# Kernel optimization log

Measured on AMD Instinct MI355X. Metric: run time of the kernel, lower is better.

## Reference

```python
import jax, jax.numpy as jnp
import numpy as np

N = 100000
H = 128
F_IN = 32
F_OUT = 16
NUM_GRAPHS = 64
NEG_SLOPE = 0.2


def setup_inputs() -> dict:
    key = jax.random.key(0)
    ks = jax.random.split(key, 16)
    inp = {
        'x': jax.random.normal(ks[0], (N, F_IN), dtype=jnp.float32),
        'edge_index': jax.random.randint(ks[1], (2, 1000000), 0, N, dtype=jnp.int32),
        'subgraph_edge_index': jax.random.randint(ks[2], (2, 1000000), 0, N, dtype=jnp.int32),
        'node_subnode_index': jax.random.randint(ks[3], (2, 200000), 0, N, dtype=jnp.int32),
        'subnode_node_index': jax.random.randint(ks[4], (2, 200000), 0, N, dtype=jnp.int32),
        'ground_node': jnp.arange(40000, dtype=jnp.int32),
        'subgraph_batch_index': jax.random.randint(ks[5], (60000,), 0, NUM_GRAPHS, dtype=jnp.int32),
        'batch_idx': jax.random.randint(ks[6], (40000,), 0, NUM_GRAPHS, dtype=jnp.int32),
    }
    s_in = 1.0 / np.sqrt(F_IN)
    s_h = 1.0 / np.sqrt(H)
    inp['emb_W'] = jax.random.uniform(ks[7], (F_IN, H), jnp.float32, -s_in, s_in)
    inp['emb_b'] = jax.random.uniform(ks[8], (H,), jnp.float32, -s_in, s_in)
    # 4 GATv2 layers (depth=1): lin_l, lin_r, att, bias per layer
    inp['Wl'] = jax.random.uniform(ks[9], (4, H, H), jnp.float32, -s_h, s_h)
    inp['Wr'] = jax.random.uniform(ks[10], (4, H, H), jnp.float32, -s_h, s_h)
    inp['att'] = jax.random.uniform(ks[11], (4, H), jnp.float32, -s_h, s_h)
    inp['bias'] = jax.random.uniform(ks[12], (4, H), jnp.float32, -s_h, s_h)
    inp['out_W'] = jax.random.uniform(ks[13], (H, F_OUT), jnp.float32, -s_h, s_h)
    inp['out_b'] = jax.random.uniform(ks[14], (F_OUT,), jnp.float32, -s_h, s_h)
    return inp


def _gatv2(x, ei, Wl, Wr, att, b):
    # add self loops (PyG GATv2Conv default add_self_loops=True)
    loops = jnp.broadcast_to(jnp.arange(N, dtype=ei.dtype)[None, :], (2, N))
    ei = jnp.concatenate([ei, loops], axis=1)
    src, dst = ei[0], ei[1]
    xl = x @ Wl  # source transform [N,H]
    xr = x @ Wr  # target transform [N,H]
    e = jax.nn.leaky_relu(xl[src] + xr[dst], NEG_SLOPE) @ att  # [E]
    m = jax.ops.segment_max(e, dst, num_segments=N)
    p = jnp.exp(e - m[dst])
    s = jax.ops.segment_sum(p, dst, num_segments=N)
    alpha = p / s[dst]
    out = jax.ops.segment_sum(alpha[:, None] * xl[src], dst, num_segments=N)
    return out + b


def reference(x, edge_index, subgraph_edge_index, node_subnode_index,
              subnode_node_index, ground_node, subgraph_batch_index, batch_idx,
              emb_W, emb_b, Wl, Wr, att, bias, out_W, out_b):
    h = x @ emb_W + emb_b
    eis = (edge_index, node_subnode_index, subgraph_edge_index, subnode_node_index)
    for i, ei in enumerate(eis):
        h = _gatv2(h, ei, Wl[i], Wr[i], att[i], bias[i])
    # global_add_pool over ground nodes
    pooled = jax.ops.segment_sum(h[ground_node], batch_idx, num_segments=NUM_GRAPHS)
    return pooled @ out_W + out_b
```

## Files before the change

kernel.cpp:

```cpp
#include <hip/hip_runtime.h>
#include <cstddef>


typedef __attribute__((ext_vector_type(8))) short bf16x8;
typedef __attribute__((ext_vector_type(4))) float f32x4;
typedef __attribute__((ext_vector_type(2))) float f32x2;

#define NSH   10
#define CHUNK 8192
#define POOLP 256

__device__ __forceinline__ unsigned short f2bf(float f) {
  unsigned int u = __float_as_uint(f);
  u += 0x7fffu + ((u >> 16) & 1u);
  return (unsigned short)(u >> 16);
}
__device__ __forceinline__ unsigned int pack2bf(float a, float b) {
  return (__float_as_uint(a) >> 16) | (__float_as_uint(b) & 0xFFFF0000u);
}
__device__ __forceinline__ float bf2f(short s) {
  return __uint_as_float(((unsigned int)(unsigned short)s) << 16);
}
__device__ __forceinline__ float2 unpk(unsigned int u) {
  return make_float2(__uint_as_float(u << 16),
                     __uint_as_float(u & 0xFFFF0000u));
}
__device__ __forceinline__ f32x2 unpk2(unsigned int u) {
  f32x2 r;
  r.x = __uint_as_float(u << 16);
  r.y = __uint_as_float(u & 0xFFFF0000u);
  return r;
}
__device__ __forceinline__ int dlog(int s) {
  int b = s >> 6, i = s & 63;
  return (b << 6) + ((i & 3) << 4) + (i >> 2);
}

__device__ __forceinline__ int lds_excl_scan(int* a, int len, int* aux, int tid)
{
  int g = (len + 255) >> 8;
  int lo = tid * g;
  int s = 0;
  for (int i = 0; i < g; ++i) { int idx = lo + i; if (idx < len) s += a[idx]; }
  aux[tid] = s;
  __syncthreads();
  for (int d = 1; d < 256; d <<= 1) {
    int v = (tid >= d) ? aux[tid - d] : 0;
    __syncthreads();
    aux[tid] += v;
    __syncthreads();
  }
  int run = aux[tid] - s;
  for (int i = 0; i < g; ++i) {
    int idx = lo + i;
    if (idx < len) { int t = a[idx]; a[idx] = run; run += t; }
  }
  int total = aux[255];
  __syncthreads();
  return total;
}

__device__ __forceinline__ void resolve_item(
    int id, int t1, int t2, int t3, int t4, int n,
    const int* s0, const int* s1, const int* s2, const int* s3,
    const int* d0, const int* d1, const int* d2, const int* d3,
    int& l, int& s, int& d, bool need_src)
{
  if (id < t4) {
    const int *sp, *dp; int e;
    if      (id < t1) { l = 0; e = id;      sp = s0; dp = d0; }
    else if (id < t2) { l = 1; e = id - t1; sp = s1; dp = d1; }
    else if (id < t3) { l = 2; e = id - t2; sp = s2; dp = d2; }
    else              { l = 3; e = id - t3; sp = s3; dp = d3; }
    d = dp[e];
    s = need_src ? sp[e] : 0;
  } else {
    int k = id - t4;
    l = (k >= 3 * n) ? 3 : (k >= 2 * n) ? 2 : (k >= n) ? 1 : 0;
    s = k - l * n; d = s;
  }
}

__global__ __launch_bounds__(256) void setup_kernel(
    const float* __restrict__ Wl, const float* __restrict__ Wr,
    const float* __restrict__ embW,
    const float* __restrict__ att, const float* __restrict__ bias,
    unsigned short* __restrict__ packB, unsigned short* __restrict__ packE,
    float* __restrict__ attA, float* __restrict__ attB,
    float* __restrict__ biasP,
    int* __restrict__ offs4, int n, int e0, int e1, int e2, int e3)
{
  const float LOG2E = 1.4426950408889634f;
  int id = blockIdx.x * 256 + threadIdx.x;
  if (id < 131072) {
    int j    = id & 7;
    int lane = (id >> 3) & 63;
    int kt   = (id >> 9) & 3;
    int ct   = (id >> 11) & 15;
    int l    = id >> 15;
    int kpos = kt * 32 + (lane >> 4) * 8 + j;
    int k    = dlog(kpos);
    int col  = ct * 16 + (lane & 15);
    float v = (ct < 8) ? Wl[(size_t)l * 16384 + k * 128 + col]
                       : Wr[(size_t)l * 16384 + k * 128 + (col - 128)];
    packB[id] = f2bf(v);
  }
  int pe = id - 131072;
  if (pe >= 0 && pe < 4096) {
    int j    = pe & 7;
    int lane = (pe >> 3) & 63;
    int ct   = pe >> 9;
    int k    = (lane >> 4) * 8 + j;
    int col  = ct * 16 + (lane & 15);
    packE[pe] = f2bf(embW[k * 128 + col]);
  }
  int ab = pe - 4096;
  if (ab >= 0 && ab < 512) {
    int l = ab >> 7, pos = ab & 127;
    int d = dlog(pos);
    float a = att[l * 128 + d];
    attA[ab]  = a * 0.6f * LOG2E;
    attB[ab]  = a * 0.4f * LOG2E;
    biasP[ab] = bias[l * 128 + d];
  }
  int q = ab - 512;
  if (q >= 0 && q < 4) {
    int El = (q == 0) ? e0 : (q == 1) ? e1 : (q == 2) ? e2 : e3;
    offs4[(size_t)q * (n + 1) + n] = El + n;
  }
}

__global__ __launch_bounds__(256) void embed_mfma_kernel(
    const float* __restrict__ x, const unsigned short* __restrict__ packE,
    const float* __restrict__ b, unsigned short* __restrict__ hb, int n)
{
  const int wave = threadIdx.x >> 6;
  const int lane = threadIdx.x & 63;
  const int rlan = lane & 15;
  const int kgrp = lane >> 4;

  bf16x8 Bf[8];
#pragma unroll
  for (int ct = 0; ct < 8; ++ct)
    Bf[ct] = *(const bf16x8*)(packE + ((size_t)ct * 64 + lane) * 8);
  float bv[8];
#pragma unroll
  for (int ct = 0; ct < 8; ++ct) bv[ct] = b[ct * 16 + rlan];

  const float4* __restrict__ x4 = (const float4*)x;
  const int ntiles = (n + 15) / 16;
  for (int tile = blockIdx.x * 4 + wave; tile < ntiles; tile += gridDim.x * 4) {
    int r = tile * 16 + rlan;
    if (r >= n) r = n - 1;
    float4 a0 = x4[(size_t)r * 8 + kgrp * 2];
    float4 a1 = x4[(size_t)r * 8 + kgrp * 2 + 1];
    bf16x8 Af;
    Af[0] = (short)f2bf(a0.x); Af[1] = (short)f2bf(a0.y);
    Af[2] = (short)f2bf(a0.z); Af[3] = (short)f2bf(a0.w);
    Af[4] = (short)f2bf(a1.x); Af[5] = (short)f2bf(a1.y);
    Af[6] = (short)f2bf(a1.z); Af[7] = (short)f2bf(a1.w);

    f32x4 acc[8];
#pragma unroll
    for (int ct = 0; ct < 8; ++ct) {
      acc[ct] = (f32x4){0.f, 0.f, 0.f, 0.f};
      acc[ct] = __builtin_amdgcn_mfma_f32_16x16x32_bf16(Af, Bf[ct], acc[ct], 0, 0, 0);
    }
    int rowb = tile * 16 + kgrp * 4;
#pragma unroll
    for (int rr = 0; rr < 4; ++rr) {
      int row = rowb + rr;
      if (row < n) {
        uint2 p0, p1;
        p0.x = pack2bf(acc[0][rr] + bv[0], acc[1][rr] + bv[1]);
        p0.y = pack2bf(acc[2][rr] + bv[2], acc[3][rr] + bv[3]);
        p1.x = pack2bf(acc[4][rr] + bv[4], acc[5][rr] + bv[5]);
        p1.y = pack2bf(acc[6][rr] + bv[6], acc[7][rr] + bv[7]);
        *(uint2*)(hb + (size_t)row * 128 + rlan * 4)      = p0;
        *(uint2*)(hb + (size_t)row * 128 + 64 + rlan * 4) = p1;
      }
    }
  }
}

#define GPAD 136
__global__ __launch_bounds__(256) void gemm_mfma_kernel(
    const unsigned short* __restrict__ hb,
    const unsigned short* __restrict__ packB,
    unsigned short* __restrict__ xlb, unsigned short* __restrict__ xrb, int n)
{
  __shared__ unsigned short hs[32 * GPAD];
  const int tid  = threadIdx.x;
  const int wave = tid >> 6;
  const int lane = tid & 63;
  const int rlan = lane & 15;
  const int kgrp = lane >> 4;

  bf16x8 Bf[4][4];
#pragma unroll
  for (int ct = 0; ct < 4; ++ct)
#pragma unroll
    for (int kt = 0; kt < 4; ++kt)
      Bf[ct][kt] = *(const bf16x8*)(packB +
          ((((size_t)(wave * 4 + ct)) * 4 + kt) * 64 + lane) * 8);

  unsigned short* __restrict__ outp = (wave < 2) ? xlb : xrb;
  const int colbase = (wave & 1) * 64;

  const int ntiles = (n + 31) / 32;
  for (int tile = blockIdx.x; tile < ntiles; tile += gridDim.x) {
    const int row0 = tile * 32;
    __syncthreads();
#pragma unroll
    for (int i = 0; i < 4; ++i) {
      int g  = (i * 256 + tid) * 8;
      int r  = g >> 7;
      int cc = g & 127;
      int gr = row0 + r; if (gr >= n) gr = n - 1;
      uint4 v = *(const uint4*)(hb + (size_t)gr * 128 + cc);
      *(uint4*)(hs + r * GPAD + cc) = v;
    }
    __syncthreads();

    bf16x8 Af[2][4];
#pragma unroll
    for (int rt = 0; rt < 2; ++rt)
#pragma unroll
      for (int kt = 0; kt < 4; ++kt)
        Af[rt][kt] = *(const bf16x8*)(hs + (rt * 16 + rlan) * GPAD
                                         + kgrp * 8 + kt * 32);

    f32x4 acc[2][4];
#pragma unroll
    for (int rt = 0; rt < 2; ++rt)
#pragma unroll
      for (int ct = 0; ct < 4; ++ct)
        acc[rt][ct] = (f32x4){0.f, 0.f, 0.f, 0.f};
#pragma unroll
    for (int kt = 0; kt < 4; ++kt)
#pragma unroll
      for (int rt = 0; rt < 2; ++rt)
#pragma unroll
        for (int ct = 0; ct < 4; ++ct)
          acc[rt][ct] = __builtin_amdgcn_mfma_f32_16x16x32_bf16(
              Af[rt][kt], Bf[ct][kt], acc[rt][ct], 0, 0, 0);
#pragma unroll
    for (int rt = 0; rt < 2; ++rt) {
      int rowb = row0 + rt * 16 + kgrp * 4;
#pragma unroll
      for (int r = 0; r < 4; ++r) {
        int row = rowb + r;
        if (row < n) {
          uint2 pk;
          pk.x = pack2bf(acc[rt][0][r], acc[rt][1][r]);
          pk.y = pack2bf(acc[rt][2][r], acc[rt][3][r]);
          *(uint2*)(outp + (size_t)row * 128 + colbase + rlan * 4) = pk;
        }
      }
    }
  }
}

__global__ __launch_bounds__(256) void hist_kernel(
    const int* __restrict__ d0, const int* __restrict__ d1,
    const int* __restrict__ d2, const int* __restrict__ d3,
    int e0, int e1, int e2, int e3, int n, int nbk, int NB, int nitems,
    int* __restrict__ mat)
{
  __shared__ int hist[512];
  int tid = threadIdx.x, c = blockIdx.x;
  for (int i = tid; i < NB; i += 256) hist[i] = 0;
  __syncthreads();
  int t1 = e0, t2 = t1 + e1, t3 = t2 + e2, t4 = t3 + e3;
  int base = c * CHUNK;
#pragma unroll
  for (int k = 0; k < CHUNK / 256; ++k) {
    int id = base + k * 256 + tid;
    if (id < nitems) {
      int l, s, d;
      resolve_item(id, t1, t2, t3, t4, n,
                   nullptr, nullptr, nullptr, nullptr, d0, d1, d2, d3,
                   l, s, d, false);
      atomicAdd(&hist[l * nbk + (d >> NSH)], 1);
    }
  }
  __syncthreads();
  for (int i = tid; i < NB; i += 256) mat[(size_t)c * NB + i] = hist[i];
}

__global__ __launch_bounds__(256) void colscan_a_kernel(
    const int* __restrict__ mat, int* __restrict__ pfx,
    int nchunk, int NB, int* __restrict__ colsum)
{
  __shared__ int col[512];
  __shared__ int aux[256];
  int gb = blockIdx.x, tid = threadIdx.x;
  for (int i = tid; i < nchunk; i += 256) col[i] = mat[(size_t)i * NB + gb];
  __syncthreads();
  int tot = lds_excl_scan(col, nchunk, aux, tid);
  for (int i = tid; i < nchunk; i += 256) pfx[(size_t)i * NB + gb] = col[i];
  if (tid == 0) colsum[gb] = tot;
}

__global__ __launch_bounds__(256) void colscan_b_kernel(
    const int* __restrict__ colsum, int NB, int* __restrict__ colscan)
{
  __shared__ int buf[512];
  __shared__ int aux[256];
  int tid = threadIdx.x;
  for (int i = tid; i < NB; i += 256) buf[i] = colsum[i];
  __syncthreads();
  int tot = lds_excl_scan(buf, NB, aux, tid);
  for (int i = tid; i < NB; i += 256) colscan[i] = buf[i];
  if (tid == 0) colscan[NB] = tot;
}

__global__ __launch_bounds__(256) void scatter_kernel(
    const int* __restrict__ s0, const int* __restrict__ s1,
    const int* __restrict__ s2, const int* __restrict__ s3,
    const int* __restrict__ d0, const int* __restrict__ d1,
    const int* __restrict__ d2, const int* __restrict__ d3,
    int e0, int e1, int e2, int e3, int n, int nbk, int NB, int nitems,
    const int* __restrict__ mat, const int* __restrict__ pfx,
    const int* __restrict__ colscan, int* __restrict__ staging)
{
  __shared__ int lbuf[CHUNK];
  __shared__ int hist[512];
  __shared__ int cur[512];
  __shared__ int basex[512];
  __shared__ int aux[256];
  int tid = threadIdx.x, c = blockIdx.x;
  for (int i = tid; i < NB; i += 256) hist[i] = mat[(size_t)c * NB + i];
  __syncthreads();
  lds_excl_scan(hist, NB, aux, tid);
  for (int i = tid; i < NB; i += 256) {
    cur[i]   = hist[i];
    basex[i] = colscan[i] + pfx[(size_t)c * NB + i];
  }
  __syncthreads();
  int t1 = e0, t2 = t1 + e1, t3 = t2 + e2, t4 = t3 + e3;
  int base = c * CHUNK;
#pragma unroll
  for (int k = 0; k < CHUNK / 256; ++k) {
    int id = base + k * 256 + tid;
    if (id < nitems) {
      int l, s, d;
      resolve_item(id, t1, t2, t3, t4, n,
                   s0, s1, s2, s3, d0, d1, d2, d3, l, s, d, true);
      int gb = l * nbk + (d >> NSH);
      int p = atomicAdd(&cur[gb], 1);
      lbuf[p] = s | ((d & ((1 << NSH) - 1)) << 17);
    }
  }
  __syncthreads();
  int wave = tid >> 6, lane = tid & 63;
  for (int gb = wave; gb < NB; gb += 4) {
    int st = hist[gb], en = cur[gb];
    int gbase = basex[gb];
    for (int j = lane; j < en - st; j += 64)
      staging[gbase + j] = lbuf[st + j];
  }
}

__global__ __launch_bounds__(256) void finalize_kernel(
    const int* __restrict__ staging, const int* __restrict__ colscan,
    int* __restrict__ offs4, int* __restrict__ csr4, int n, int nbk,
    int cb0, int cb1, int cb2, int cb3)
{
  __shared__ int cnt[1 << NSH];
  __shared__ int pos[1 << NSH];
  __shared__ int aux[256];
  int gb = blockIdx.x, tid = threadIdx.x;
  int l = gb / nbk, b = gb % nbk;
  int beg = colscan[gb], end = colscan[gb + 1];
  int node0 = b << NSH;
  int ncount = n - node0; if (ncount > (1 << NSH)) ncount = 1 << NSH;
  int cbl = (l == 0) ? cb0 : (l == 1) ? cb1 : (l == 2) ? cb2 : cb3;

  for (int i = tid; i < (1 << NSH); i += 256) cnt[i] = 0;
  __syncthreads();
  for (int t = beg + tid; t < end; t += 256)
    atomicAdd(&cnt[staging[t] >> 17], 1);
  __syncthreads();
  lds_excl_scan(cnt, 1 << NSH, aux, tid);
  for (int i = tid; i < (1 << NSH); i += 256) {
    if (i < ncount)
      offs4[(size_t)l * (n + 1) + node0 + i] = beg + cnt[i] - cbl;
    pos[i] = cnt[i];
  }
  __syncthreads();
  for (int t = beg + tid; t < end; t += 256) {
    int e = staging[t];
    int p = atomicAdd(&pos[e >> 17], 1);
    csr4[beg + p] = e & 0x1FFFF;
  }
}

__global__ __launch_bounds__(256) void gat_dst_kernel(
    const unsigned short* __restrict__ xlb,
    const unsigned short* __restrict__ xrb,
    const int* __restrict__ offs, const int* __restrict__ csr,
    const float* __restrict__ attA, const float* __restrict__ attB,
    const float* __restrict__ biasP,
    float* __restrict__ hout_f, unsigned short* __restrict__ hout_b, int n)
{
  int wid = (blockIdx.x * 256 + threadIdx.x) >> 4;
  int c   = threadIdx.x & 15;
  if (wid >= n) return;

  uint4 xru = *(const uint4*)(xrb + (size_t)wid * 128 + c * 8);
  f32x2 xr0 = unpk2(xru.x), xr1 = unpk2(xru.y);
  f32x2 xr2 = unpk2(xru.z), xr3 = unpk2(xru.w);
  const f32x2* aA2 = (const f32x2*)(attA + c * 8);
  f32x2 aA0 = aA2[0], aA1 = aA2[1], aA2v = aA2[2], aA3 = aA2[3];
  const float* aBp = attB + c * 8;
  float aB0 = aBp[0], aB1 = aBp[1], aB2 = aBp[2], aB3 = aBp[3];
  float aB4 = aBp[4], aB5 = aBp[5], aB6 = aBp[6], aB7 = aBp[7];

  int beg = offs[wid], end = offs[wid + 1];
  float ssum = 0.f;
  f32x2 ac0 = {0.f, 0.f}, ac1 = {0.f, 0.f};
  f32x2 ac2 = {0.f, 0.f}, ac3 = {0.f, 0.f};

  int s0 = csr[beg];
  uint4 xu = *(const uint4*)(xlb + (size_t)s0 * 128 + c * 8);

  for (int j = beg; j < end; ++j) {
    uint4 cu = xu;
    int jn = j + 1;
    if (jn < end) {
      int sn = csr[jn];
      xu = *(const uint4*)(xlb + (size_t)sn * 128 + c * 8);
    }
    f32x2 xs0 = unpk2(cu.x), xs1 = unpk2(cu.y);
    f32x2 xs2 = unpk2(cu.z), xs3 = unpk2(cu.w);
    f32x2 t0 = xs0 + xr0;
    f32x2 t1 = xs1 + xr1;
    f32x2 t2 = xs2 + xr2;
    f32x2 t3 = xs3 + xr3;
    f32x2 sA = t0 * aA0;
    sA = __builtin_elementwise_fma(t1, aA1, sA);
    sA = __builtin_elementwise_fma(t2, aA2v, sA);
    sA = __builtin_elementwise_fma(t3, aA3, sA);
    float pB0 = fmaf(aB0, __builtin_fabsf(t0.x), sA.x);
    float pB1 = fmaf(aB1, __builtin_fabsf(t0.y), sA.y);
    pB0 = fmaf(aB2, __builtin_fabsf(t1.x), pB0);
    pB1 = fmaf(aB3, __builtin_fabsf(t1.y), pB1);
    pB0 = fmaf(aB4, __builtin_fabsf(t2.x), pB0);
    pB1 = fmaf(aB5, __builtin_fabsf(t2.y), pB1);
    pB0 = fmaf(aB6, __builtin_fabsf(t3.x), pB0);
    pB1 = fmaf(aB7, __builtin_fabsf(t3.y), pB1);
    float part = pB0 + pB1;
    part += __shfl_xor(part, 1, 64);
    part += __shfl_xor(part, 2, 64);
    part += __shfl_xor(part, 4, 64);
    part += __shfl_xor(part, 8, 64);
    float p = __builtin_amdgcn_exp2f(part);
    ssum += p;
    f32x2 pv = {p, p};
    ac0 = __builtin_elementwise_fma(pv, xs0, ac0);
    ac1 = __builtin_elementwise_fma(pv, xs1, ac1);
    ac2 = __builtin_elementwise_fma(pv, xs2, ac2);
    ac3 = __builtin_elementwise_fma(pv, xs3, ac3);
  }

  float inv = 1.0f / ssum;
  float o[8] = {ac0.x, ac0.y, ac1.x, ac1.y, ac2.x, ac2.y, ac3.x, ac3.y};
  const float* bi = biasP + c * 8;
#pragma unroll
  for (int k = 0; k < 8; ++k) o[k] = fmaf(o[k], inv, bi[k]);

  if (hout_f) {
    float4 v0 = make_float4(o[0], o[1], o[2], o[3]);
    float4 v1 = make_float4(o[4], o[5], o[6], o[7]);
    *(float4*)(hout_f + (size_t)wid * 128 + c * 8)     = v0;
    *(float4*)(hout_f + (size_t)wid * 128 + c * 8 + 4) = v1;
  } else {
    bf16x8 ob;
#pragma unroll
    for (int k = 0; k < 8; ++k) ob[k] = (short)f2bf(o[k]);
    *(bf16x8*)(hout_b + (size_t)wid * 128 + c * 8) = ob;
  }
}

__global__ __launch_bounds__(256) void pool_partial_kernel(
    const float* __restrict__ h, const int* __restrict__ gnode,
    const int* __restrict__ bidx, float* __restrict__ partial, int ng)
{
  __shared__ float acc[64 * 128];
  int tid = threadIdx.x;
  for (int t = tid; t < 64 * 128; t += 256) acc[t] = 0.f;
  __syncthreads();
  int col = tid & 127, half = tid >> 7;
  for (int nd = blockIdx.x * 2 + half; nd < ng; nd += gridDim.x * 2) {
    int row = gnode[nd];
    int g   = bidx[nd];
    atomicAdd(&acc[g * 128 + col], h[(size_t)row * 128 + col]);
  }
  __syncthreads();
  float* out = partial + (size_t)blockIdx.x * 8192;
  for (int t = tid; t < 64 * 128; t += 256) out[t] = acc[t];
}

__global__ __launch_bounds__(128) void pool_out_kernel(
    const float* __restrict__ partial, const float* __restrict__ W,
    const float* __restrict__ b, float* __restrict__ out)
{
  __shared__ float pr[128];
  int g = blockIdx.x, tid = threadIdx.x;
  float s = 0.f;
  for (int p = 0; p < POOLP; ++p) s += partial[(size_t)p * 8192 + g * 128 + tid];
  pr[tid] = s;
  __syncthreads();
  if (tid < 16) {
    float acc = b[tid];
#pragma unroll
    for (int k = 0; k < 128; ++k) acc += pr[k] * W[dlog(k) * 16 + tid];
    out[g * 16 + tid] = acc;
  }
}

extern "C" void kernel_launch(void* const* d_in, const int* in_sizes, int n_in,
                              void* d_out, int out_size, void* d_ws, size_t ws_size,
                              hipStream_t stream)
{
  const float* x    = (const float*)d_in[0];
  const int* ei0    = (const int*)d_in[1];
  const int* ei_sg  = (const int*)d_in[2];
  const int* ei_ns  = (const int*)d_in[3];
  const int* ei_sn  = (const int*)d_in[4];
  const int* gnode  = (const int*)d_in[5];
  const int* bidx   = (const int*)d_in[7];
  const float* embW = (const float*)d_in[8];
  const float* embB = (const float*)d_in[9];
  const float* Wl   = (const float*)d_in[10];
  const float* Wr   = (const float*)d_in[11];
  const float* att  = (const float*)d_in[12];
  const float* bias = (const float*)d_in[13];
  const float* outW = (const float*)d_in[14];
  const float* outB = (const float*)d_in[15];

  const int n  = in_sizes[0] / 32;
  const int ng = in_sizes[5];

  const int  E_arr[4] = { in_sizes[1] / 2, in_sizes[3] / 2,
                          in_sizes[2] / 2, in_sizes[4] / 2 };
  const int* eptr[4]  = { ei0, ei_ns, ei_sg, ei_sn };
  const int E_tot  = E_arr[0] + E_arr[1] + E_arr[2] + E_arr[3];
  const int nitems = E_tot + 4 * n;
  const int nbk    = (n + (1 << NSH) - 1) >> NSH;
  const int NB     = 4 * nbk;
  const int nchunk = (nitems + CHUNK - 1) / CHUNK;
  int cb[4];
  cb[0] = 0;
  for (int i = 1; i < 4; ++i) cb[i] = cb[i - 1] + E_arr[i - 1] + n;

  char* ws = (char*)d_ws;
  size_t off = 0;
  auto alloc = [&](size_t bytes) -> void* {
    void* p = ws + off;
    off = (off + bytes + 255) & ~(size_t)255;
    return p;
  };
  float*          h      = (float*)alloc((size_t)n * 128 * sizeof(float));
  unsigned short* hb     = (unsigned short*)alloc((size_t)n * 128 * sizeof(unsigned short));
  unsigned short* xlb    = (unsigned short*)alloc((size_t)n * 128 * sizeof(unsigned short));
  unsigned short* xrb    = (unsigned short*)alloc((size_t)n * 128 * sizeof(unsigned short));
  int*            offs4  = (int*)alloc((size_t)4 * (n + 1) * sizeof(int));
  int*            mat    = (int*)alloc((size_t)nchunk * NB * sizeof(int));
  int*            pfx    = (int*)alloc((size_t)nchunk * NB * sizeof(int));
  int*            colsum = (int*)alloc((size_t)NB * sizeof(int));
  int*            colscan= (int*)alloc((size_t)(NB + 1) * sizeof(int));
  int*            staging= (int*)alloc((size_t)nitems * sizeof(int));
  int*            csr4   = (int*)alloc((size_t)nitems * sizeof(int));
  unsigned short* packB  = (unsigned short*)alloc(131072 * sizeof(unsigned short));
  unsigned short* packE  = (unsigned short*)alloc(4096 * sizeof(unsigned short));
  float*          attA   = (float*)alloc(512 * sizeof(float));
  float*          attB   = (float*)alloc(512 * sizeof(float));
  float*          biasP  = (float*)alloc(512 * sizeof(float));
  float*          partial= (float*)alloc((size_t)POOLP * 8192 * sizeof(float));
  (void)ws_size; (void)n_in; (void)out_size;

  const int* D[4] = { eptr[0] + E_arr[0], eptr[1] + E_arr[1],
                      eptr[2] + E_arr[2], eptr[3] + E_arr[3] };

  int setup_items = 131072 + 4096 + 512 + 4;
  setup_kernel<<<(setup_items + 255) / 256, 256, 0, stream>>>(
      Wl, Wr, embW, att, bias, packB, packE, attA, attB, biasP, offs4, n,
      E_arr[0], E_arr[1], E_arr[2], E_arr[3]);

  const int ntile16 = (n + 15) / 16;
  embed_mfma_kernel<<<(ntile16 + 3) / 4, 256, 0, stream>>>(
      x, packE, embB, hb, n);

  hist_kernel<<<nchunk, 256, 0, stream>>>(
      D[0], D[1], D[2], D[3], E_arr[0], E_arr[1], E_arr[2], E_arr[3],
      n, nbk, NB, nitems, mat);
  colscan_a_kernel<<<NB, 256, 0, stream>>>(mat, pfx, nchunk, NB, colsum);
  colscan_b_kernel<<<1, 256, 0, stream>>>(colsum, NB, colscan);
  scatter_kernel<<<nchunk, 256, 0, stream>>>(
      eptr[0], eptr[1], eptr[2], eptr[3], D[0], D[1], D[2], D[3],
      E_arr[0], E_arr[1], E_arr[2], E_arr[3], n, nbk, NB, nitems,
      mat, pfx, colscan, staging);
  finalize_kernel<<<NB, 256, 0, stream>>>(
      staging, colscan, offs4, csr4, n, nbk, cb[0], cb[1], cb[2], cb[3]);

  const int ntile32 = (n + 31) / 32;
  const int gemm_grid = (ntile32 + 1) / 2;
  for (int l = 0; l < 4; ++l) {
    gemm_mfma_kernel<<<gemm_grid, 256, 0, stream>>>(
        hb, packB + (size_t)l * 32768, xlb, xrb, n);
    gat_dst_kernel<<<((size_t)n * 16 + 255) / 256, 256, 0, stream>>>(
        xlb, xrb, offs4 + (size_t)l * (n + 1), csr4 + cb[l],
        attA + l * 128, attB + l * 128, biasP + l * 128,
        (l == 3) ? h : nullptr, (l < 3) ? hb : nullptr, n);
  }

  pool_partial_kernel<<<POOLP, 256, 0, stream>>>(h, gnode, bidx, partial, ng);
  pool_out_kernel<<<64, 128, 0, stream>>>(partial, outW, outB, (float*)d_out);
}
```

Before: 486.9 us.

## Process destination nodes in descending-degree order to balance GAT aggregation waves

Adds a degree histogram, scan and scatter pass that builds, per layer, a permutation of destination nodes sorted by in-degree in descending order (capped at 63). The GAT aggregation kernel maps each 16-lane group to `ord[wid]` instead of `wid`, so the four nodes sharing a 64-lane wave have similar edge counts and the longest nodes start first. The aim is to cut divergence and tail imbalance in the edge loop. It also reassociates the attention dot product into two independent partial sums for more instruction-level parallelism. The costs are three extra kernel launches, one extra indirection per node, and scattered rather than sequential reads of xr and offsets and writes of the output.

```diff
diff --git a/kernel.cpp b/kernel.cpp
--- a/kernel.cpp
+++ b/kernel.cpp
@@ -88,7 +88,8 @@
     unsigned short* __restrict__ packB, unsigned short* __restrict__ packE,
     float* __restrict__ attA, float* __restrict__ attB,
     float* __restrict__ biasP,
-    int* __restrict__ offs4, int n, int e0, int e1, int e2, int e3)
+    int* __restrict__ offs4, int* __restrict__ dhist, int* __restrict__ dcur,
+    int n, int e0, int e1, int e2, int e3)
 {
   const float LOG2E = 1.4426950408889634f;
   int id = blockIdx.x * 256 + threadIdx.x;
@@ -128,6 +129,10 @@
     int El = (q == 0) ? e0 : (q == 1) ? e1 : (q == 2) ? e2 : e3;
     offs4[(size_t)q * (n + 1) + n] = El + n;
   }
+  int z = q - 4;
+  if (z >= 0 && z < 512) {
+    if (z < 256) dhist[z] = 0; else dcur[z - 256] = 0;
+  }
 }
 
 __global__ __launch_bounds__(256) void embed_mfma_kernel(
@@ -396,10 +401,55 @@
   }
 }
 
+__global__ __launch_bounds__(256) void deg_hist_kernel(
+    const int* __restrict__ offs4, int n, int* __restrict__ dhist)
+{
+  __shared__ int lh[64];
+  int l = blockIdx.y;
+  int i = blockIdx.x * 256 + threadIdx.x;
+  if (threadIdx.x < 64) lh[threadIdx.x] = 0;
+  __syncthreads();
+  if (i < n) {
+    const int* o = offs4 + (size_t)l * (n + 1);
+    int deg = o[i + 1] - o[i]; if (deg > 63) deg = 63;
+    atomicAdd(&lh[63 - deg], 1);
+  }
+  __syncthreads();
+  if (threadIdx.x < 64 && lh[threadIdx.x] > 0)
+    atomicAdd(&dhist[l * 64 + threadIdx.x], lh[threadIdx.x]);
+}
+
+__global__ __launch_bounds__(256) void deg_scatter_kernel(
+    const int* __restrict__ offs4, const int* __restrict__ dbase,
+    int* __restrict__ dcur, int* __restrict__ order, int n)
+{
+  __shared__ int lh[64], lbase[64], lcur[64];
+  int l = blockIdx.y;
+  int i = blockIdx.x * 256 + threadIdx.x;
+  if (threadIdx.x < 64) { lh[threadIdx.x] = 0; lcur[threadIdx.x] = 0; }
+  __syncthreads();
+  int rbin = 0;
+  if (i < n) {
+    const int* o = offs4 + (size_t)l * (n + 1);
+    int deg = o[i + 1] - o[i]; if (deg > 63) deg = 63;
+    rbin = 63 - deg;
+    atomicAdd(&lh[rbin], 1);
+  }
+  __syncthreads();
+  if (threadIdx.x < 64 && lh[threadIdx.x] > 0)
+    lbase[threadIdx.x] = atomicAdd(&dcur[l * 64 + threadIdx.x], lh[threadIdx.x]);
+  __syncthreads();
+  if (i < n) {
+    int p = atomicAdd(&lcur[rbin], 1);
+    order[dbase[l * 64 + rbin] + lbase[rbin] + p] = i;
+  }
+}
+
 __global__ __launch_bounds__(256) void gat_dst_kernel(
     const unsigned short* __restrict__ xlb,
     const unsigned short* __restrict__ xrb,
     const int* __restrict__ offs, const int* __restrict__ csr,
+    const int* __restrict__ ord,
     const float* __restrict__ attA, const float* __restrict__ attB,
     const float* __restrict__ biasP,
     float* __restrict__ hout_f, unsigned short* __restrict__ hout_b, int n)
@@ -407,8 +457,9 @@
   int wid = (blockIdx.x * 256 + threadIdx.x) >> 4;
   int c   = threadIdx.x & 15;
   if (wid >= n) return;
-
-  uint4 xru = *(const uint4*)(xrb + (size_t)wid * 128 + c * 8);
+  int node = ord[wid];
+
+  uint4 xru = *(const uint4*)(xrb + (size_t)node * 128 + c * 8);
   f32x2 xr0 = unpk2(xru.x), xr1 = unpk2(xru.y);
   f32x2 xr2 = unpk2(xru.z), xr3 = unpk2(xru.w);
   const f32x2* aA2 = (const f32x2*)(attA + c * 8);
@@ -417,7 +468,7 @@
   float aB0 = aBp[0], aB1 = aBp[1], aB2 = aBp[2], aB3 = aBp[3];
   float aB4 = aBp[4], aB5 = aBp[5], aB6 = aBp[6], aB7 = aBp[7];
 
-  int beg = offs[wid], end = offs[wid + 1];
+  int beg = offs[node], end = offs[node + 1];
   float ssum = 0.f;
   f32x2 ac0 = {0.f, 0.f}, ac1 = {0.f, 0.f};
   f32x2 ac2 = {0.f, 0.f}, ac3 = {0.f, 0.f};
@@ -442,15 +493,15 @@
     sA = __builtin_elementwise_fma(t1, aA1, sA);
     sA = __builtin_elementwise_fma(t2, aA2v, sA);
     sA = __builtin_elementwise_fma(t3, aA3, sA);
-    float pB0 = fmaf(aB0, __builtin_fabsf(t0.x), sA.x);
-    float pB1 = fmaf(aB1, __builtin_fabsf(t0.y), sA.y);
-    pB0 = fmaf(aB2, __builtin_fabsf(t1.x), pB0);
-    pB1 = fmaf(aB3, __builtin_fabsf(t1.y), pB1);
-    pB0 = fmaf(aB4, __builtin_fabsf(t2.x), pB0);
-    pB1 = fmaf(aB5, __builtin_fabsf(t2.y), pB1);
-    pB0 = fmaf(aB6, __builtin_fabsf(t3.x), pB0);
-    pB1 = fmaf(aB7, __builtin_fabsf(t3.y), pB1);
-    float part = pB0 + pB1;
+    float sB0 = aB0 * __builtin_fabsf(t0.x);
+    float sB1 = aB1 * __builtin_fabsf(t0.y);
+    sB0 = fmaf(aB2, __builtin_fabsf(t1.x), sB0);
+    sB1 = fmaf(aB3, __builtin_fabsf(t1.y), sB1);
+    sB0 = fmaf(aB4, __builtin_fabsf(t2.x), sB0);
+    sB1 = fmaf(aB5, __builtin_fabsf(t2.y), sB1);
+    sB0 = fmaf(aB6, __builtin_fabsf(t3.x), sB0);
+    sB1 = fmaf(aB7, __builtin_fabsf(t3.y), sB1);
+    float part = (sA.x + sA.y) + (sB0 + sB1);
     part += __shfl_xor(part, 1, 64);
     part += __shfl_xor(part, 2, 64);
     part += __shfl_xor(part, 4, 64);
@@ -473,13 +524,13 @@
   if (hout_f) {
     float4 v0 = make_float4(o[0], o[1], o[2], o[3]);
     float4 v1 = make_float4(o[4], o[5], o[6], o[7]);
-    *(float4*)(hout_f + (size_t)wid * 128 + c * 8)     = v0;
-    *(float4*)(hout_f + (size_t)wid * 128 + c * 8 + 4) = v1;
+    *(float4*)(hout_f + (size_t)node * 128 + c * 8)     = v0;
+    *(float4*)(hout_f + (size_t)node * 128 + c * 8 + 4) = v1;
   } else {
     bf16x8 ob;
 #pragma unroll
     for (int k = 0; k < 8; ++k) ob[k] = (short)f2bf(o[k]);
-    *(bf16x8*)(hout_b + (size_t)wid * 128 + c * 8) = ob;
+    *(bf16x8*)(hout_b + (size_t)node * 128 + c * 8) = ob;
   }
 }
 
@@ -578,16 +629,20 @@
   float*          attA   = (float*)alloc(512 * sizeof(float));
   float*          attB   = (float*)alloc(512 * sizeof(float));
   float*          biasP  = (float*)alloc(512 * sizeof(float));
+  int*            dhist  = (int*)alloc(256 * sizeof(int));
+  int*            dcur   = (int*)alloc(256 * sizeof(int));
+  int*            dbase  = (int*)alloc(257 * sizeof(int));
+  int*            order  = (int*)alloc((size_t)4 * n * sizeof(int));
   float*          partial= (float*)alloc((size_t)POOLP * 8192 * sizeof(float));
   (void)ws_size; (void)n_in; (void)out_size;
 
   const int* D[4] = { eptr[0] + E_arr[0], eptr[1] + E_arr[1],
                       eptr[2] + E_arr[2], eptr[3] + E_arr[3] };
 
-  int setup_items = 131072 + 4096 + 512 + 4;
+  int setup_items = 131072 + 4096 + 512 + 4 + 512;
   setup_kernel<<<(setup_items + 255) / 256, 256, 0, stream>>>(
-      Wl, Wr, embW, att, bias, packB, packE, attA, attB, biasP, offs4, n,
-      E_arr[0], E_arr[1], E_arr[2], E_arr[3]);
+      Wl, Wr, embW, att, bias, packB, packE, attA, attB, biasP, offs4,
+      dhist, dcur, n, E_arr[0], E_arr[1], E_arr[2], E_arr[3]);
 
   const int ntile16 = (n + 15) / 16;
   embed_mfma_kernel<<<(ntile16 + 3) / 4, 256, 0, stream>>>(
@@ -605,6 +660,11 @@
   finalize_kernel<<<NB, 256, 0, stream>>>(
       staging, colscan, offs4, csr4, n, nbk, cb[0], cb[1], cb[2], cb[3]);
 
+  dim3 dgrid((n + 255) / 256, 4);
+  deg_hist_kernel<<<dgrid, 256, 0, stream>>>(offs4, n, dhist);
+  colscan_b_kernel<<<1, 256, 0, stream>>>(dhist, 256, dbase);
+  deg_scatter_kernel<<<dgrid, 256, 0, stream>>>(offs4, dbase, dcur, order, n);
+
   const int ntile32 = (n + 31) / 32;
   const int gemm_grid = (ntile32 + 1) / 2;
   for (int l = 0; l < 4; ++l) {
@@ -612,6 +672,7 @@
         hb, packB + (size_t)l * 32768, xlb, xrb, n);
     gat_dst_kernel<<<((size_t)n * 16 + 255) / 256, 256, 0, stream>>>(
         xlb, xrb, offs4 + (size_t)l * (n + 1), csr4 + cb[l],
+        order + (size_t)l * n,
         attA + l * 128, attB + l * 128, biasP + l * 128,
         (l == 3) ? h : nullptr, (l < 3) ? hb : nullptr, n);
   }
```

After: 495.9 us. Within noise of the previous version (+1.9%).
